# Optimization experiments

Measured on AMD Instinct MI355X. Metric: run time of the kernel, lower is better.

Reference implementation:

```python
import jax, jax.numpy as jnp
import numpy as np

B, NP, ED, D, H, P, SP, TP, NF, L = 8, 784, 1024, 512, 8, 16, 14, 8, 16, 4
NPAT = SP * SP * TP  # 1568 total patches
FF = 4 * D
DH = D // H
OUT_D = P * P * 3 * 2  # 1536


def _ln(x, w, b):
    m = x.mean(-1, keepdims=True)
    v = ((x - m) ** 2).mean(-1, keepdims=True)
    return (x - m) / jnp.sqrt(v + 1e-5) * w + b


def _mha(q_in, kv_in, qkv_w, qkv_b, out_w, out_b):
    wq, wk, wv = jnp.split(qkv_w, 3, 0)
    bq, bk, bv = jnp.split(qkv_b, 3, 0)
    def heads(t):
        b, s, _ = t.shape
        return t.reshape(b, s, H, DH).transpose(0, 2, 1, 3)
    q = heads(q_in @ wq.T + bq)
    k = heads(kv_in @ wk.T + bk)
    v = heads(kv_in @ wv.T + bv)
    a = jax.nn.softmax(jnp.einsum('bhqd,bhkd->bhqk', q, k) / jnp.sqrt(jnp.float32(DH)), axis=-1)
    o = jnp.einsum('bhqk,bhkd->bhqd', a, v).transpose(0, 2, 1, 3).reshape(q_in.shape[0], -1, D)
    return o @ out_w.T + out_b


def _pos_embed():
    pos = jnp.arange(NPAT, dtype=jnp.float32)[:, None]
    div = jnp.exp(jnp.arange(0, D, 2, dtype=jnp.float32) * (-np.log(10000.0) / D))
    pe = jnp.zeros((NPAT, D), jnp.float32)
    pe = pe.at[:, 0::2].set(jnp.sin(pos * div)).at[:, 1::2].set(jnp.cos(pos * div))
    return pe


def setup_inputs() -> dict:
    key = jax.random.key(0)
    ks = jax.random.split(key, 26)
    s = 0.02
    inp = {
        'z': jax.random.normal(ks[0], (B, NP, ED), jnp.float32),
        'mask_pred': jax.random.randint(ks[1], (B, NP), 0, NPAT, jnp.int32),
        'embed_w': jax.random.normal(ks[2], (D, ED)) * s,
        'embed_b': jnp.zeros((D,)),
        'sa_qkv_w': jax.random.normal(ks[3], (L, 3 * D, D)) * s,
        'sa_qkv_b': jnp.zeros((L, 3 * D)),
        'sa_out_w': jax.random.normal(ks[4], (L, D, D)) * s,
        'sa_out_b': jnp.zeros((L, D)),
        'ca_qkv_w': jax.random.normal(ks[5], (L, 3 * D, D)) * s,
        'ca_qkv_b': jnp.zeros((L, 3 * D)),
        'ca_out_w': jax.random.normal(ks[6], (L, D, D)) * s,
        'ca_out_b': jnp.zeros((L, D)),
        'ff1_w': jax.random.normal(ks[7], (L, FF, D)) * s,
        'ff1_b': jnp.zeros((L, FF)),
        'ff2_w': jax.random.normal(ks[8], (L, D, FF)) * s,
        'ff2_b': jnp.zeros((L, D)),
        'ln1_w': jnp.ones((L, D)), 'ln1_b': jnp.zeros((L, D)),
        'ln2_w': jnp.ones((L, D)), 'ln2_b': jnp.zeros((L, D)),
        'ln3_w': jnp.ones((L, D)), 'ln3_b': jnp.zeros((L, D)),
        'norm_w': jnp.ones((D,)), 'norm_b': jnp.zeros((D,)),
        'pred_w': jax.random.normal(ks[9], (OUT_D, D)) * s,
        'pred_b': jnp.zeros((OUT_D,)),
    }
    return inp


def reference(z, mask_pred, embed_w, embed_b, sa_qkv_w, sa_qkv_b, sa_out_w, sa_out_b,
              ca_qkv_w, ca_qkv_b, ca_out_w, ca_out_b, ff1_w, ff1_b, ff2_w, ff2_b,
              ln1_w, ln1_b, ln2_w, ln2_b, ln3_w, ln3_b, norm_w, norm_b, pred_w, pred_b):
    x = z @ embed_w.T + embed_b  # [B, NP, D]
    mem = jnp.broadcast_to(_pos_embed()[None], (z.shape[0], NPAT, D))
    for l in range(L):  # TransformerDecoderLayer, norm_first=False, eval (dropout off)
        x = _ln(x + _mha(x, x, sa_qkv_w[l], sa_qkv_b[l], sa_out_w[l], sa_out_b[l]), ln1_w[l], ln1_b[l])
        x = _ln(x + _mha(x, mem, ca_qkv_w[l], ca_qkv_b[l], ca_out_w[l], ca_out_b[l]), ln2_w[l], ln2_b[l])
        ff = jax.nn.gelu(x @ ff1_w[l].T + ff1_b[l], approximate=False) @ ff2_w[l].T + ff2_b[l]
        x = _ln(x + ff, ln3_w[l], ln3_b[l])
    x = _ln(x, norm_w, norm_b)
    pred = x @ pred_w.T + pred_b  # [B, NP, P*P*3*2]
    # vectorized reconstruct_frames: scatter patch tiles into frame tensor
    patches = pred.reshape(B, NP, 2, 3, P, P)
    t_idx = mask_pred // (SP * SP)
    s_idx = mask_pred % (SP * SP)
    h_idx = s_idx // SP
    w_idx = s_idx % SP
    frame_idx = t_idx[:, :, None] * 2 + jnp.arange(2)  # [B, NP, 2]
    b_idx = jnp.arange(B)[:, None, None]
    frames = jnp.zeros((B, NF, 3, SP, P, SP, P), pred.dtype)
    frames = frames.at[b_idx, frame_idx, :, h_idx[:, :, None], :, w_idx[:, :, None], :].set(patches)
    return frames.reshape(B, NF, 3, SP * P, SP * P)
```

## Files before the change

kernel.cpp:

```cpp
#include <hip/hip_runtime.h>
#include <hip/hip_bf16.h>
#include <math.h>

#define B_    8
#define NP_   784
#define ED_   1024
#define D_    512
#define H_    8
#define DH_   64
#define NPAT_ 1568
#define FF_   2048
#define L_    4
#define OUTD_ 1536
#define M_    (B_ * NP_)

#define NT_SA 13
#define NT_CA 25

typedef __attribute__((ext_vector_type(8))) short bf16x8;
typedef __attribute__((ext_vector_type(4))) float f32x4;

static __device__ inline void split_bf16(float x, unsigned short& h, unsigned short& l)
{
    unsigned bits = __float_as_uint(x);
    h = (unsigned short)(bits >> 16);
    float r = x - __uint_as_float(bits & 0xFFFF0000u);
    l = (unsigned short)(__float_as_uint(r) >> 16);
}

__global__ __launch_bounds__(256) void conv_w_kernel(
    const float* __restrict__ src, size_t lss, int N, int K,
    short* __restrict__ dst, size_t lsd)
{
    const int t  = threadIdx.x;
    const int l  = blockIdx.y;
    const int gs = blockIdx.x * 4 + (t >> 6);
    const int m  = t & 63;
    const int NB16 = N >> 4;
    const int kb = gs / NB16;
    const int ns = gs % NB16;

    const float* p = src + (size_t)l * lss + (size_t)(ns * 16 + (m & 15)) * K
                   + kb * 32 + (m >> 4) * 8;
    float4 a0 = *(const float4*)p;
    float4 a1 = *(const float4*)(p + 4);
    float xv[8] = {a0.x, a0.y, a0.z, a0.w, a1.x, a1.y, a1.z, a1.w};
    union { short s_[8]; bf16x8 v; } hi, lo;
#pragma unroll
    for (int e = 0; e < 8; e++) {
        unsigned short hh, ll;
        split_bf16(xv[e], hh, ll);
        hi.s_[e] = (short)hh; lo.s_[e] = (short)ll;
    }
    short* o = dst + (size_t)l * lsd + (size_t)gs * 1024 + m * 8;
    *(bf16x8*)o         = hi.v;
    *(bf16x8*)(o + 512) = lo.v;
}

template <int ACT, int PW>
__global__ __launch_bounds__(256, 2) void gemm_mfma_kernel(
    const float* __restrict__ A, int lda,
    const float* __restrict__ W, int ldw,
    const short* __restrict__ wsp, int NB16, int cOff,
    const float* __restrict__ bias,
    float* __restrict__ C, int ldc, size_t cstride,
    int M, int N, int K, int KC)
{
    __shared__ short sAh[8 * 512];
    __shared__ short sAl[8 * 512];
    __shared__ short sBh[8 * 512];
    __shared__ short sBl[8 * 512];

    const int t    = threadIdx.x;
    const int lane = t & 63;
    const int wid  = t >> 6;
    const int wr   = wid >> 1;
    const int wc   = wid & 1;
    const int bm   = blockIdx.y * 128;
    const int bn   = blockIdx.x * 128;
    const int kBeg = blockIdx.z * KC;
    C += (size_t)blockIdx.z * cstride;

    const int srow  = t >> 1;
    const int shalf = t & 1;

    int arow = bm + srow; if (arow >= M) arow = M - 1;
    const float* aptr = A + (size_t)arow * lda + shalf * 16;
    const float* wptr = (PW == 0) ? (W + (size_t)(bn + srow) * ldw + shalf * 16) : nullptr;

    const int wbase = (srow >> 4) * 512 + (srow & 15) * 8 + shalf * 256;

    f32x4 acc[4][4];
    {
        const int col = bn + wc * 64 + (lane & 15);
#pragma unroll
        for (int j = 0; j < 4; j++) {
            float bv = (blockIdx.z == 0) ? bias[col + j * 16] : 0.0f;
            for (int i = 0; i < 4; i++) acc[i][j] = (f32x4)(bv);
        }
    }

    for (int k0 = kBeg; k0 < kBeg + KC; k0 += 32) {
        float4 av[4];
#pragma unroll
        for (int q = 0; q < 4; q++) av[q] = *(const float4*)(aptr + k0 + q * 4);

        float4 wv[4];
        bf16x8 bh0, bh1, bl0, bl1;
        if constexpr (PW == 0) {
#pragma unroll
            for (int q = 0; q < 4; q++) wv[q] = *(const float4*)(wptr + k0 + q * 4);
        } else {
            const short* gb = wsp + ((size_t)(k0 >> 5) * NB16 + (bn >> 4) + cOff) * 1024
                            + (t >> 5) * 1024 + (t & 31) * 16;
            bh0 = *(const bf16x8*)gb;
            bh1 = *(const bf16x8*)(gb + 8);
            bl0 = *(const bf16x8*)(gb + 512);
            bl1 = *(const bf16x8*)(gb + 520);
        }
        __syncthreads();

        {
            union { short s[16]; bf16x8 v[2]; } ah, al;
#pragma unroll
            for (int q = 0; q < 4; q++) {
                const float* ap = (const float*)&av[q];
#pragma unroll
                for (int e = 0; e < 4; e++) {
                    unsigned short hh, ll;
                    split_bf16(ap[e], hh, ll);
                    ah.s[q * 4 + e] = (short)hh; al.s[q * 4 + e] = (short)ll;
                }
            }
            *(bf16x8*)&sAh[wbase]       = ah.v[0];
            *(bf16x8*)&sAh[wbase + 128] = ah.v[1];
            *(bf16x8*)&sAl[wbase]       = al.v[0];
            *(bf16x8*)&sAl[wbase + 128] = al.v[1];
        }
        if constexpr (PW == 0) {
            union { short s[16]; bf16x8 v[2]; } wh, wl;
#pragma unroll
            for (int q = 0; q < 4; q++) {
                const float* wp = (const float*)&wv[q];
#pragma unroll
                for (int e = 0; e < 4; e++) {
                    unsigned short hh, ll;
                    split_bf16(wp[e], hh, ll);
                    wh.s[q * 4 + e] = (short)hh; wl.s[q * 4 + e] = (short)ll;
                }
            }
            *(bf16x8*)&sBh[wbase]       = wh.v[0];
            *(bf16x8*)&sBh[wbase + 128] = wh.v[1];
            *(bf16x8*)&sBl[wbase]       = wl.v[0];
            *(bf16x8*)&sBl[wbase + 128] = wl.v[1];
        } else {
            *(bf16x8*)&sBh[t * 16]     = bh0;
            *(bf16x8*)&sBh[t * 16 + 8] = bh1;
            *(bf16x8*)&sBl[t * 16]     = bl0;
            *(bf16x8*)&sBl[t * 16 + 8] = bl1;
        }
        __syncthreads();

        bf16x8 ahf[4], alf[4], bhf[4], blf[4];
#pragma unroll
        for (int i = 0; i < 4; i++) {
            int sa = (wr * 4 + i) * 512 + lane * 8;
            ahf[i] = *(const bf16x8*)&sAh[sa];
            alf[i] = *(const bf16x8*)&sAl[sa];
        }
#pragma unroll
        for (int j = 0; j < 4; j++) {
            int sb = (wc * 4 + j) * 512 + lane * 8;
            bhf[j] = *(const bf16x8*)&sBh[sb];
            blf[j] = *(const bf16x8*)&sBl[sb];
        }
#pragma unroll
        for (int i = 0; i < 4; i++)
#pragma unroll
            for (int j = 0; j < 4; j++) {
                acc[i][j] = __builtin_amdgcn_mfma_f32_16x16x32_bf16(ahf[i], bhf[j], acc[i][j], 0, 0, 0);
                acc[i][j] = __builtin_amdgcn_mfma_f32_16x16x32_bf16(ahf[i], blf[j], acc[i][j], 0, 0, 0);
                acc[i][j] = __builtin_amdgcn_mfma_f32_16x16x32_bf16(alf[i], bhf[j], acc[i][j], 0, 0, 0);
            }
    }

#pragma unroll
    for (int i = 0; i < 4; i++) {
        int row0 = bm + wr * 64 + i * 16 + ((lane >> 4) << 2);
#pragma unroll
        for (int r = 0; r < 4; r++) {
            int row = row0 + r;
            if (row < M) {
#pragma unroll
                for (int j = 0; j < 4; j++) {
                    int col = bn + wc * 64 + j * 16 + (lane & 15);
                    float v = acc[i][j][r];
                    if (ACT == 1) v = 0.5f * v * (1.0f + erff(v * 0.70710678118654752f));
                    C[(size_t)row * ldc + col] = v;
                }
            }
        }
    }
}

static inline void launch_gemm(bool pw, bool act, dim3 grid, hipStream_t st,
    const float* A, int lda, const float* W, int ldw,
    const short* wsp, int NB16, int cOff, const float* bias,
    float* C, int ldc, size_t cstride, int M, int N, int K, int KC)
{
    if (pw) {
        if (act) gemm_mfma_kernel<1,1><<<grid,256,0,st>>>(A,lda,W,ldw,wsp,NB16,cOff,bias,C,ldc,cstride,M,N,K,KC);
        else     gemm_mfma_kernel<0,1><<<grid,256,0,st>>>(A,lda,W,ldw,wsp,NB16,cOff,bias,C,ldc,cstride,M,N,K,KC);
    } else {
        if (act) gemm_mfma_kernel<1,0><<<grid,256,0,st>>>(A,lda,W,ldw,wsp,NB16,cOff,bias,C,ldc,cstride,M,N,K,KC);
        else     gemm_mfma_kernel<0,0><<<grid,256,0,st>>>(A,lda,W,ldw,wsp,NB16,cOff,bias,C,ldc,cstride,M,N,K,KC);
    }
}

template <int MODE>
__global__ __launch_bounds__(256) void conv_kv_kernel(
    const float* __restrict__ src, int ld, size_t bstride, int rows,
    short* __restrict__ out, int NT)
{
    const int t    = threadIdx.x;
    const int half = blockIdx.x & 1;
    const int tile = blockIdx.x >> 1;
    const int bh   = blockIdx.y;
    const int b    = bh >> 3;
    const int h    = bh & 7;
    const int s    = half * 4 + (t >> 6);
    const int m    = t & 63;

    float xv[8];
    if (MODE == 0) {
        int kv = tile * 64 + (s & 3) * 16 + (m & 15);
        if (kv >= rows) kv = rows - 1;
        int dh = (s >> 2) * 32 + (m >> 4) * 8;
        const float* p = src + (size_t)b * bstride + (size_t)kv * ld + h * 64 + dh;
        float4 a0 = *(const float4*)p;
        float4 a1 = *(const float4*)(p + 4);
        xv[0] = a0.x; xv[1] = a0.y; xv[2] = a0.z; xv[3] = a0.w;
        xv[4] = a1.x; xv[5] = a1.y; xv[6] = a1.z; xv[7] = a1.w;
    } else {
        int dh  = (s & 3) * 16 + (m & 15);
        int kv0 = tile * 64 + (s >> 2) * 32 + (m >> 4) * 8;
        const float* p = src + (size_t)b * bstride + h * 64 + dh;
#pragma unroll
        for (int j = 0; j < 8; j++) {
            int kv = kv0 + j; if (kv >= rows) kv = rows - 1;
            xv[j] = p[(size_t)kv * ld];
        }
    }
    union { short s_[8]; bf16x8 v; } hi, lo;
#pragma unroll
    for (int e = 0; e < 8; e++) {
        unsigned short hh, ll;
        split_bf16(xv[e], hh, ll);
        hi.s_[e] = (short)hh; lo.s_[e] = (short)ll;
    }
    short* o = out + ((size_t)bh * NT + tile) * 8192 + s * 512 + m * 8;
    *(bf16x8*)o          = hi.v;
    *(bf16x8*)(o + 4096) = lo.v;
}

__global__ __launch_bounds__(256, 3) void attn_mfma2_kernel(
    const float* __restrict__ Q, int ldq, size_t qStride,
    const short* __restrict__ kconv, const short* __restrict__ vconv,
    int bhB,
    float* __restrict__ O,
    int qLen, int kvLen, int NT)
{
    __shared__ short sK[8192];
    __shared__ short sV[8192];
    __shared__ short sP[4][2048];

    const int t    = threadIdx.x;
    const int lane = t & 63;
    const int wid  = t >> 6;
    const int g    = lane >> 4;
    const int l15  = lane & 15;
    const int qt   = blockIdx.x;
    const int h    = blockIdx.y;
    const int b    = blockIdx.z;
    const int hoff = h * 64;
    const int bh   = b * bhB + h;

    int qrow = qt * 64 + wid * 16 + l15;
    int qcl  = qrow < qLen ? qrow : qLen - 1;
    const float* qp = Q + (size_t)b * qStride + (size_t)qcl * ldq + hoff + g * 8;
    bf16x8 qh[2], ql[2];
#pragma unroll
    for (int ks = 0; ks < 2; ks++) {
        float4 x0 = *(const float4*)(qp + ks * 32);
        float4 x1 = *(const float4*)(qp + ks * 32 + 4);
        float xv[8] = {x0.x, x0.y, x0.z, x0.w, x1.x, x1.y, x1.z, x1.w};
        union { short s[8]; bf16x8 v; } hi, lo;
#pragma unroll
        for (int e = 0; e < 8; e++) {
            unsigned short hh, ll;
            split_bf16(xv[e] * 0.125f, hh, ll);
            hi.s[e] = (short)hh; lo.s[e] = (short)ll;
        }
        qh[ks] = hi.v; ql[ks] = lo.v;
    }

    f32x4 o[4];
#pragma unroll
    for (int f = 0; f < 4; f++) o[f] = (f32x4)(0.0f);
    float m = -1e30f, lsum = 0.0f;

    char* const phw = (char*)&sP[wid][0];
    char* const plw = phw + 2048;

    for (int tile = 0; tile < NT; ++tile) {
        const short* kt = kconv + ((size_t)bh * NT + tile) * 8192;
        const short* vt = vconv + ((size_t)bh * NT + tile) * 8192;
        bf16x8 kreg[4], vreg[4];
#pragma unroll
        for (int i = 0; i < 4; i++) {
            kreg[i] = *(const bf16x8*)(kt + i * 2048 + t * 8);
            vreg[i] = *(const bf16x8*)(vt + i * 2048 + t * 8);
        }
        __syncthreads();
#pragma unroll
        for (int i = 0; i < 4; i++) {
            *(bf16x8*)&sK[i * 2048 + t * 8] = kreg[i];
            *(bf16x8*)&sV[i * 2048 + t * 8] = vreg[i];
        }
        __syncthreads();

        f32x4 s[4];
#pragma unroll
        for (int f = 0; f < 4; f++) s[f] = (f32x4)(0.0f);
#pragma unroll
        for (int f = 0; f < 4; f++)
#pragma unroll
            for (int ks = 0; ks < 2; ks++) {
                int off = (ks * 4 + f) * 512 + lane * 8;
                bf16x8 kh8 = *(const bf16x8*)&sK[off];
                bf16x8 kl8 = *(const bf16x8*)&sK[off + 4096];
                s[f] = __builtin_amdgcn_mfma_f32_16x16x32_bf16(kh8, qh[ks], s[f], 0, 0, 0);
                s[f] = __builtin_amdgcn_mfma_f32_16x16x32_bf16(kh8, ql[ks], s[f], 0, 0, 0);
                s[f] = __builtin_amdgcn_mfma_f32_16x16x32_bf16(kl8, qh[ks], s[f], 0, 0, 0);
            }

        int kv0 = tile * 64;
        float tmax = -1e30f;
#pragma unroll
        for (int f = 0; f < 4; f++)
#pragma unroll
            for (int r = 0; r < 4; r++) {
                float sv = s[f][r];
                int kvg = kv0 + 16 * f + g * 4 + r;
                sv = (kvg < kvLen) ? sv : -1e30f;
                s[f][r] = sv;
                tmax = fmaxf(tmax, sv);
            }
        tmax = fmaxf(tmax, __shfl_xor(tmax, 16));
        tmax = fmaxf(tmax, __shfl_xor(tmax, 32));
        float mnew  = fmaxf(m, tmax);
        float alpha = __expf(m - mnew);
        m = mnew;
        lsum *= alpha;

#pragma unroll
        for (int f = 0; f < 4; f++) {
            float p0 = __expf(s[f][0] - mnew);
            float p1 = __expf(s[f][1] - mnew);
            float p2 = __expf(s[f][2] - mnew);
            float p3 = __expf(s[f][3] - mnew);
            lsum += (p0 + p1) + (p2 + p3);
            unsigned short h0,h1,h2,h3, l0,l1,l2,l3;
            split_bf16(p0, h0, l0); split_bf16(p1, h1, l1);
            split_bf16(p2, h2, l2); split_bf16(p3, h3, l3);
            uint2 uh, ul;
            uh.x = (unsigned)h0 | ((unsigned)h1 << 16);
            uh.y = (unsigned)h2 | ((unsigned)h3 << 16);
            ul.x = (unsigned)l0 | ((unsigned)l1 << 16);
            ul.y = (unsigned)l2 | ((unsigned)l3 << 16);
            int wa = (l15 * 128 + f * 32 + g * 8) ^ ((l15 & 7) << 4);
            *(uint2*)(phw + wa) = uh;
            *(uint2*)(plw + wa) = ul;
        }

        {
            float a0 = __shfl(alpha, g * 4 + 0);
            float a1 = __shfl(alpha, g * 4 + 1);
            float a2 = __shfl(alpha, g * 4 + 2);
            float a3 = __shfl(alpha, g * 4 + 3);
#pragma unroll
            for (int f = 0; f < 4; f++) {
                o[f][0] *= a0; o[f][1] *= a1; o[f][2] *= a2; o[f][3] *= a3;
            }
        }

#pragma unroll
        for (int ks = 0; ks < 2; ks++) {
            int pa = (l15 * 128 + ks * 64 + g * 16) ^ ((l15 & 7) << 4);
            bf16x8 p_h = *(const bf16x8*)(phw + pa);
            bf16x8 p_l = *(const bf16x8*)(plw + pa);
#pragma unroll
            for (int f = 0; f < 4; f++) {
                int off = (ks * 4 + f) * 512 + lane * 8;
                bf16x8 vh8 = *(const bf16x8*)&sV[off];
                bf16x8 vl8 = *(const bf16x8*)&sV[off + 4096];
                o[f] = __builtin_amdgcn_mfma_f32_16x16x32_bf16(p_h, vh8, o[f], 0, 0, 0);
                o[f] = __builtin_amdgcn_mfma_f32_16x16x32_bf16(p_h, vl8, o[f], 0, 0, 0);
                o[f] = __builtin_amdgcn_mfma_f32_16x16x32_bf16(p_l, vh8, o[f], 0, 0, 0);
            }
        }
    }

    lsum += __shfl_xor(lsum, 16);
    lsum += __shfl_xor(lsum, 32);
    float linv = 1.0f / lsum;
    float lr0 = __shfl(linv, g * 4 + 0);
    float lr1 = __shfl(linv, g * 4 + 1);
    float lr2 = __shfl(linv, g * 4 + 2);
    float lr3 = __shfl(linv, g * 4 + 3);
    float lr[4] = {lr0, lr1, lr2, lr3};

    int row0 = qt * 64 + wid * 16 + g * 4;
#pragma unroll
    for (int r = 0; r < 4; r++) {
        int row = row0 + r;
        if (row < qLen) {
            float* op = O + ((size_t)b * qLen + row) * 512 + hoff + l15;
#pragma unroll
            for (int f = 0; f < 4; f++)
                op[f * 16] = o[f][r] * lr[r];
        }
    }
}

__global__ __launch_bounds__(256) void ln_kernel(
    const float* __restrict__ a, int nParts, size_t pstride,
    const float* __restrict__ res,
    const float* __restrict__ w, const float* __restrict__ bb,
    float* __restrict__ out, int M)
{
    const int wid  = threadIdx.x >> 6;
    const int lane = threadIdx.x & 63;
    const int row  = blockIdx.x * 4 + wid;
    if (row >= M) return;

    const size_t base = (size_t)row * 512 + lane * 8;
    float4 x0 = *(const float4*)(a + base);
    float4 x1 = *(const float4*)(a + base + 4);
    float v[8] = {x0.x, x0.y, x0.z, x0.w, x1.x, x1.y, x1.z, x1.w};
    for (int p = 1; p < nParts; p++) {
        const float* pp = a + (size_t)p * pstride + base;
        float4 r0 = *(const float4*)pp;
        float4 r1 = *(const float4*)(pp + 4);
        v[0] += r0.x; v[1] += r0.y; v[2] += r0.z; v[3] += r0.w;
        v[4] += r1.x; v[5] += r1.y; v[6] += r1.z; v[7] += r1.w;
    }
    if (res) {
        const float* rp = res + base;
        float4 r0 = *(const float4*)rp;
        float4 r1 = *(const float4*)(rp + 4);
        v[0] += r0.x; v[1] += r0.y; v[2] += r0.z; v[3] += r0.w;
        v[4] += r1.x; v[5] += r1.y; v[6] += r1.z; v[7] += r1.w;
    }
    float sum = 0.f, sq = 0.f;
#pragma unroll
    for (int j = 0; j < 8; j++) { sum += v[j]; sq = fmaf(v[j], v[j], sq); }
#pragma unroll
    for (int off = 1; off < 64; off <<= 1) {
        sum += __shfl_xor(sum, off);
        sq  += __shfl_xor(sq, off);
    }
    float mean = sum * (1.0f / 512.0f);
    float var  = sq * (1.0f / 512.0f) - mean * mean;
    float rstd = 1.0f / sqrtf(var + 1e-5f);

    const float* wp = w + lane * 8;
    const float* bp = bb + lane * 8;
    float ov[8];
#pragma unroll
    for (int j = 0; j < 8; j++) ov[j] = (v[j] - mean) * rstd * wp[j] + bp[j];
    float* op = out + base;
    *(float4*)op       = make_float4(ov[0], ov[1], ov[2], ov[3]);
    *(float4*)(op + 4) = make_float4(ov[4], ov[5], ov[6], ov[7]);
}

__global__ __launch_bounds__(256) void posembed_kernel(float* __restrict__ mem)
{
    int idx = blockIdx.x * 256 + threadIdx.x;
    if (idx >= NPAT_ * 256) return;
    int pos = idx >> 8;
    int i   = idx & 255;
    float div = expf((float)(2 * i) * (-9.21034037197618f / 512.0f));
    float ang = (float)pos * div;
    mem[(size_t)pos * 512 + 2 * i]     = sinf(ang);
    mem[(size_t)pos * 512 + 2 * i + 1] = cosf(ang);
}

__global__ __launch_bounds__(256) void winner_kernel(
    const int* __restrict__ mask, int* __restrict__ winner)
{
    int idx = blockIdx.x * 256 + threadIdx.x;
    if (idx >= B_ * NP_) return;
    int b = idx / NP_;
    atomicMax(&winner[b * NPAT_ + mask[idx]], idx % NP_);
}

__global__ __launch_bounds__(256) void scatter_kernel(
    const float* __restrict__ pred, const int* __restrict__ mask,
    const int* __restrict__ winner, float* __restrict__ out)
{
    int idx = blockIdx.x * 256 + threadIdx.x;
    if (idx >= B_ * NP_ * OUTD_) return;
    int e  = idx % OUTD_;
    int bp = idx / OUTD_;
    int p  = bp % NP_;
    int b  = bp / NP_;
    int mv = mask[b * NP_ + p];
    if (winner[b * NPAT_ + mv] != p) return;

    int f  = e / 768;
    int rm = e % 768;
    int c  = rm / 256;
    int r2 = rm % 256;
    int ph = r2 / 16;
    int pw = r2 % 16;
    int tt = mv / 196;
    int ss = mv % 196;
    int hi = ss / 14;
    int wi = ss % 14;

    size_t dst = ((size_t)((b * 16 + tt * 2 + f) * 3 + c)) * (224 * 224)
               + (size_t)(hi * 16 + ph) * 224 + (wi * 16 + pw);
    out[dst] = pred[(size_t)bp * OUTD_ + e];
}

extern "C" void kernel_launch(void* const* d_in, const int* in_sizes, int n_in,
                              void* d_out, int out_size, void* d_ws, size_t ws_size,
                              hipStream_t stream)
{
    const float* z       = (const float*)d_in[0];
    const int*   mask    = (const int*)d_in[1];
    const float* embed_w = (const float*)d_in[2];
    const float* embed_b = (const float*)d_in[3];
    const float* sa_qkv_w = (const float*)d_in[4];
    const float* sa_qkv_b = (const float*)d_in[5];
    const float* sa_out_w = (const float*)d_in[6];
    const float* sa_out_b = (const float*)d_in[7];
    const float* ca_qkv_w = (const float*)d_in[8];
    const float* ca_qkv_b = (const float*)d_in[9];
    const float* ca_out_w = (const float*)d_in[10];
    const float* ca_out_b = (const float*)d_in[11];
    const float* ff1_w = (const float*)d_in[12];
    const float* ff1_b = (const float*)d_in[13];
    const float* ff2_w = (const float*)d_in[14];
    const float* ff2_b = (const float*)d_in[15];
    const float* ln1_w = (const float*)d_in[16];
    const float* ln1_b = (const float*)d_in[17];
    const float* ln2_w = (const float*)d_in[18];
    const float* ln2_b = (const float*)d_in[19];
    const float* ln3_w = (const float*)d_in[20];
    const float* ln3_b = (const float*)d_in[21];
    const float* norm_w = (const float*)d_in[22];
    const float* norm_b = (const float*)d_in[23];
    const float* pred_w = (const float*)d_in[24];
    const float* pred_b = (const float*)d_in[25];

    float* ws  = (float*)d_ws;
    float* x   = ws;
    float* y   = x   + (size_t)M_ * 512;
    float* qkv = y   + (size_t)M_ * 2048;
    float* att = qkv + (size_t)M_ * 1536;
    float* mem = att + (size_t)M_ * 512;
    float* ckv = mem + (size_t)NPAT_ * 512;
    int* winner = (int*)(ckv + (size_t)NPAT_ * 1024);

    short* kconvSA = (short*)y;
    short* vconvSA = kconvSA + (size_t)64 * NT_SA * 8192;
    short* kconvCA = vconvSA + (size_t)64 * NT_SA * 8192;
    short* vconvCA = kconvCA + (size_t)8 * NT_CA * 8192;

    short* wsb = (short*)(winner + B_ * NPAT_);
    const size_t o_embed = 0;
    const size_t o_saqkv = o_embed + 1048576;
    const size_t o_saout = o_saqkv + 4ull * 1572864;
    const size_t o_caqkv = o_saout + 4ull * 524288;
    const size_t o_caout = o_caqkv + 4ull * 1572864;
    const size_t o_ff1   = o_caout + 4ull * 524288;
    const size_t o_ff2   = o_ff1 + 4ull * 2097152;
    const size_t o_pred  = o_ff2 + 4ull * 2097152;
    const size_t wsplit_shorts = o_pred + 1572864;
    const size_t need = (size_t)((char*)wsb - (char*)d_ws) + wsplit_shorts * 2;
    const bool pw = ws_size >= need;

    const size_t PS = (size_t)M_ * 512;

    if (pw) {
        conv_w_kernel<<<dim3(256, 1), 256, 0, stream>>>(embed_w, 0, 512, 1024, wsb + o_embed, 0);
        conv_w_kernel<<<dim3(384, 4), 256, 0, stream>>>(sa_qkv_w, 1536 * 512, 1536, 512, wsb + o_saqkv, 1572864);
        conv_w_kernel<<<dim3(128, 4), 256, 0, stream>>>(sa_out_w, 512 * 512, 512, 512, wsb + o_saout, 524288);
        conv_w_kernel<<<dim3(384, 4), 256, 0, stream>>>(ca_qkv_w, 1536 * 512, 1536, 512, wsb + o_caqkv, 1572864);
        conv_w_kernel<<<dim3(128, 4), 256, 0, stream>>>(ca_out_w, 512 * 512, 512, 512, wsb + o_caout, 524288);
        conv_w_kernel<<<dim3(512, 4), 256, 0, stream>>>(ff1_w, 2048 * 512, 2048, 512, wsb + o_ff1, 2097152);
        conv_w_kernel<<<dim3(512, 4), 256, 0, stream>>>(ff2_w, 512 * 2048, 512, 2048, wsb + o_ff2, 2097152);
        conv_w_kernel<<<dim3(384, 1), 256, 0, stream>>>(pred_w, 0, 1536, 512, wsb + o_pred, 0);
    }

    posembed_kernel<<<NPAT_, 256, 0, stream>>>(mem);

    launch_gemm(pw, false, dim3(4, 49, 1), stream, z, ED_, embed_w, ED_,
                wsb + o_embed, 32, 0, embed_b, x, 512, 0, M_, 512, ED_, ED_);

    for (int l = 0; l < L_; l++) {
        const float* saw = sa_qkv_w + (size_t)l * 1536 * 512;
        const float* sab = sa_qkv_b + (size_t)l * 1536;
        const float* sow = sa_out_w + (size_t)l * 512 * 512;
        const float* sob = sa_out_b + (size_t)l * 512;
        const float* caw = ca_qkv_w + (size_t)l * 1536 * 512;
        const float* cab = ca_qkv_b + (size_t)l * 1536;
        const float* cow = ca_out_w + (size_t)l * 512 * 512;
        const float* cob = ca_out_b + (size_t)l * 512;
        const float* f1w = ff1_w + (size_t)l * 2048 * 512;
        const float* f1b = ff1_b + (size_t)l * 2048;
        const float* f2w = ff2_w + (size_t)l * 512 * 2048;
        const float* f2b = ff2_b + (size_t)l * 512;

        launch_gemm(pw, false, dim3(12, 49, 1), stream, x, 512, saw, 512,
                    wsb + o_saqkv + (size_t)l * 1572864, 96, 0, sab, qkv, 1536, 0, M_, 1536, 512, 512);
        conv_kv_kernel<0><<<dim3(NT_SA * 2, 64), 256, 0, stream>>>(
            qkv + 512, 1536, (size_t)NP_ * 1536, NP_, kconvSA, NT_SA);
        conv_kv_kernel<1><<<dim3(NT_SA * 2, 64), 256, 0, stream>>>(
            qkv + 1024, 1536, (size_t)NP_ * 1536, NP_, vconvSA, NT_SA);
        attn_mfma2_kernel<<<dim3(13, H_, B_), 256, 0, stream>>>(
            qkv, 1536, (size_t)NP_ * 1536, kconvSA, vconvSA, 8,
            att, NP_, NP_, NT_SA);
        launch_gemm(pw, false, dim3(4, 49, 2), stream, att, 512, sow, 512,
                    wsb + o_saout + (size_t)l * 524288, 32, 0, sob, qkv, 512, PS, M_, 512, 512, 256);
        ln_kernel<<<(M_ + 3) / 4, 256, 0, stream>>>(
            qkv, 2, PS, x, ln1_w + l * 512, ln1_b + l * 512, x, M_);

        launch_gemm(pw, false, dim3(4, 49, 1), stream, x, 512, caw, 512,
                    wsb + o_caqkv + (size_t)l * 1572864, 96, 0, cab, qkv, 512, 0, M_, 512, 512, 512);
        launch_gemm(pw, false, dim3(8, 13, 1), stream, mem, 512, caw + 512 * 512, 512,
                    wsb + o_caqkv + (size_t)l * 1572864, 96, 32, cab + 512, ckv, 1024, 0, NPAT_, 1024, 512, 512);
        conv_kv_kernel<0><<<dim3(NT_CA * 2, 8), 256, 0, stream>>>(
            ckv, 1024, (size_t)0, NPAT_, kconvCA, NT_CA);
        conv_kv_kernel<1><<<dim3(NT_CA * 2, 8), 256, 0, stream>>>(
            ckv + 512, 1024, (size_t)0, NPAT_, vconvCA, NT_CA);
        attn_mfma2_kernel<<<dim3(13, H_, B_), 256, 0, stream>>>(
            qkv, 512, (size_t)NP_ * 512, kconvCA, vconvCA, 0,
            att, NP_, NPAT_, NT_CA);
        launch_gemm(pw, false, dim3(4, 49, 2), stream, att, 512, cow, 512,
                    wsb + o_caout + (size_t)l * 524288, 32, 0, cob, qkv, 512, PS, M_, 512, 512, 256);
        ln_kernel<<<(M_ + 3) / 4, 256, 0, stream>>>(
            qkv, 2, PS, x, ln2_w + l * 512, ln2_b + l * 512, x, M_);

        launch_gemm(pw, true, dim3(16, 49, 1), stream, x, 512, f1w, 512,
                    wsb + o_ff1 + (size_t)l * 2097152, 128, 0, f1b, y, 2048, 0, M_, 2048, 512, 512);
        launch_gemm(pw, false, dim3(4, 49, 4), stream, y, 2048, f2w, 2048,
                    wsb + o_ff2 + (size_t)l * 2097152, 32, 0, f2b, qkv, 512, PS, M_, 512, 2048, 512);
        ln_kernel<<<(M_ + 3) / 4, 256, 0, stream>>>(
            qkv, 4, PS, x, ln3_w + l * 512, ln3_b + l * 512, x, M_);
    }

    ln_kernel<<<(M_ + 3) / 4, 256, 0, stream>>>(x, 1, 0, nullptr, norm_w, norm_b, x, M_);
    launch_gemm(pw, false, dim3(12, 49, 1), stream, x, 512, pred_w, 512,
                wsb + o_pred, 96, 0, pred_b, qkv, 1536, 0, M_, 1536, 512, 512);

    hipMemsetAsync(d_out, 0, (size_t)out_size * sizeof(float), stream);
    hipMemsetAsync(winner, 0xFF, (size_t)B_ * NPAT_ * sizeof(int), stream);
    winner_kernel<<<(B_ * NP_ + 255) / 256, 256, 0, stream>>>(mask, winner);
    scatter_kernel<<<(B_ * NP_ * OUTD_ + 255) / 256, 256, 0, stream>>>(
        qkv, mask, winner, (float*)d_out);
}
```

Baseline: 2.129 ms.

## Drop P low-part MFMA, remap attention grid for XCD locality, add setprio

The attention kernel stops splitting the softmax probabilities into hi/lo bf16 parts. It keeps only a truncated bf16 P, sums the truncated values into lsum, and removes one of the three MFMAs per PV step and half the P shared memory. The grid becomes a flat 1D index so that blocks sharing a batch (self-attention) or a head (cross-attention) land on the same XCD for K/V cache reuse. It also raises the occupancy hint and wraps the MFMA sections in s_setprio. This lowers precision of the P·V product, which risks accuracy drift against an fp32 reference.

Measured after the change: 1.978 ms. -7.1%, faster.

```diff
diff --git a/kernel.cpp b/kernel.cpp
--- a/kernel.cpp
+++ b/kernel.cpp
@@ -263,27 +263,32 @@
     *(bf16x8*)(o + 4096) = lo.v;
 }
 
-__global__ __launch_bounds__(256, 3) void attn_mfma2_kernel(
+__global__ __launch_bounds__(256, 4) void attn_mfma3_kernel(
     const float* __restrict__ Q, int ldq, size_t qStride,
     const short* __restrict__ kconv, const short* __restrict__ vconv,
-    int bhB,
+    int saMode,
     float* __restrict__ O,
     int qLen, int kvLen, int NT)
 {
     __shared__ short sK[8192];
     __shared__ short sV[8192];
-    __shared__ short sP[4][2048];
+    __shared__ short sP[4][1024];
 
     const int t    = threadIdx.x;
     const int lane = t & 63;
     const int wid  = t >> 6;
     const int g    = lane >> 4;
     const int l15  = lane & 15;
-    const int qt   = blockIdx.x;
-    const int h    = blockIdx.y;
-    const int b    = blockIdx.z;
+
+    const int id  = blockIdx.x;
+    const int xcd = id & 7;
+    const int sbl = id >> 3;
+    const int qt  = sbl % 13;
+    const int jj  = sbl / 13;
+    const int b   = saMode ? xcd : jj;
+    const int h   = saMode ? jj : xcd;
+    const int bh  = saMode ? (b * 8 + h) : h;
     const int hoff = h * 64;
-    const int bh   = b * bhB + h;
 
     int qrow = qt * 64 + wid * 16 + l15;
     int qcl  = qrow < qLen ? qrow : qLen - 1;
@@ -310,7 +315,6 @@
     float m = -1e30f, lsum = 0.0f;
 
     char* const phw = (char*)&sP[wid][0];
-    char* const plw = phw + 2048;
 
     for (int tile = 0; tile < NT; ++tile) {
         const short* kt = kconv + ((size_t)bh * NT + tile) * 8192;
@@ -332,6 +336,7 @@
         f32x4 s[4];
 #pragma unroll
         for (int f = 0; f < 4; f++) s[f] = (f32x4)(0.0f);
+        __builtin_amdgcn_s_setprio(1);
 #pragma unroll
         for (int f = 0; f < 4; f++)
 #pragma unroll
@@ -343,6 +348,7 @@
                 s[f] = __builtin_amdgcn_mfma_f32_16x16x32_bf16(kh8, ql[ks], s[f], 0, 0, 0);
                 s[f] = __builtin_amdgcn_mfma_f32_16x16x32_bf16(kl8, qh[ks], s[f], 0, 0, 0);
             }
+        __builtin_amdgcn_s_setprio(0);
 
         int kv0 = tile * 64;
         float tmax = -1e30f;
@@ -365,22 +371,18 @@
 
 #pragma unroll
         for (int f = 0; f < 4; f++) {
-            float p0 = __expf(s[f][0] - mnew);
-            float p1 = __expf(s[f][1] - mnew);
-            float p2 = __expf(s[f][2] - mnew);
-            float p3 = __expf(s[f][3] - mnew);
-            lsum += (p0 + p1) + (p2 + p3);
-            unsigned short h0,h1,h2,h3, l0,l1,l2,l3;
-            split_bf16(p0, h0, l0); split_bf16(p1, h1, l1);
-            split_bf16(p2, h2, l2); split_bf16(p3, h3, l3);
-            uint2 uh, ul;
-            uh.x = (unsigned)h0 | ((unsigned)h1 << 16);
-            uh.y = (unsigned)h2 | ((unsigned)h3 << 16);
-            ul.x = (unsigned)l0 | ((unsigned)l1 << 16);
-            ul.y = (unsigned)l2 | ((unsigned)l3 << 16);
+            unsigned hb[4];
+#pragma unroll
+            for (int r = 0; r < 4; r++) {
+                float p = __expf(s[f][r] - mnew);
+                hb[r] = __float_as_uint(p) >> 16;
+                lsum += __uint_as_float(hb[r] << 16);
+            }
+            uint2 uh;
+            uh.x = hb[0] | (hb[1] << 16);
+            uh.y = hb[2] | (hb[3] << 16);
             int wa = (l15 * 128 + f * 32 + g * 8) ^ ((l15 & 7) << 4);
             *(uint2*)(phw + wa) = uh;
-            *(uint2*)(plw + wa) = ul;
         }
 
         {
@@ -394,11 +396,11 @@
             }
         }
 
+        __builtin_amdgcn_s_setprio(1);
 #pragma unroll
         for (int ks = 0; ks < 2; ks++) {
             int pa = (l15 * 128 + ks * 64 + g * 16) ^ ((l15 & 7) << 4);
             bf16x8 p_h = *(const bf16x8*)(phw + pa);
-            bf16x8 p_l = *(const bf16x8*)(plw + pa);
 #pragma unroll
             for (int f = 0; f < 4; f++) {
                 int off = (ks * 4 + f) * 512 + lane * 8;
@@ -406,9 +408,9 @@
                 bf16x8 vl8 = *(const bf16x8*)&sV[off + 4096];
                 o[f] = __builtin_amdgcn_mfma_f32_16x16x32_bf16(p_h, vh8, o[f], 0, 0, 0);
                 o[f] = __builtin_amdgcn_mfma_f32_16x16x32_bf16(p_h, vl8, o[f], 0, 0, 0);
-                o[f] = __builtin_amdgcn_mfma_f32_16x16x32_bf16(p_l, vh8, o[f], 0, 0, 0);
-            }
-        }
+            }
+        }
+        __builtin_amdgcn_s_setprio(0);
     }
 
     lsum += __shfl_xor(lsum, 16);
@@ -630,8 +632,8 @@
             qkv + 512, 1536, (size_t)NP_ * 1536, NP_, kconvSA, NT_SA);
         conv_kv_kernel<1><<<dim3(NT_SA * 2, 64), 256, 0, stream>>>(
             qkv + 1024, 1536, (size_t)NP_ * 1536, NP_, vconvSA, NT_SA);
-        attn_mfma2_kernel<<<dim3(13, H_, B_), 256, 0, stream>>>(
-            qkv, 1536, (size_t)NP_ * 1536, kconvSA, vconvSA, 8,
+        attn_mfma3_kernel<<<832, 256, 0, stream>>>(
+            qkv, 1536, (size_t)NP_ * 1536, kconvSA, vconvSA, 1,
             att, NP_, NP_, NT_SA);
         launch_gemm(pw, false, dim3(4, 49, 2), stream, att, 512, sow, 512,
                     wsb + o_saout + (size_t)l * 524288, 32, 0, sob, qkv, 512, PS, M_, 512, 512, 256);
@@ -646,7 +648,7 @@
             ckv, 1024, (size_t)0, NPAT_, kconvCA, NT_CA);
         conv_kv_kernel<1><<<dim3(NT_CA * 2, 8), 256, 0, stream>>>(
             ckv + 512, 1024, (size_t)0, NPAT_, vconvCA, NT_CA);
-        attn_mfma2_kernel<<<dim3(13, H_, B_), 256, 0, stream>>>(
+        attn_mfma3_kernel<<<832, 256, 0, stream>>>(
             qkv, 512, (size_t)NP_ * 512, kconvCA, vconvCA, 0,
             att, NP_, NPAT_, NT_CA);
         launch_gemm(pw, false, dim3(4, 49, 2), stream, att, 512, cow, 512,
```
